# Kernel tuning notes

Hardware: AMD Instinct MI355X
Metric: run time of the kernel (lower is better)

Reference implementation:

```python
import jax, jax.numpy as jnp
import numpy as np

NUM_HEADS = 8
WINDOW_SIZE = 4
DIM = 384


def setup_inputs() -> dict:
    key = jax.random.key(0)
    k_x, k_qkv, k_pw, k_pb = jax.random.split(key, 4)
    B, N, C = 8, 16384, DIM
    x = jax.random.normal(k_x, (B, N, C), dtype=jnp.float32)
    # torch nn.Linear weights are [out_features, in_features]
    W_qkv = jax.random.normal(k_qkv, (3 * C, C), dtype=jnp.float32) * (1.0 / np.sqrt(C))
    W_proj = jax.random.normal(k_pw, (C, C), dtype=jnp.float32) * (1.0 / np.sqrt(C))
    b_proj = jax.random.normal(k_pb, (C,), dtype=jnp.float32) * 0.01
    return {"x": x, "W_qkv": W_qkv, "W_proj": W_proj, "b_proj": b_proj}


def reference(x, W_qkv, W_proj, b_proj):
    B, N, C = x.shape
    H = int(round(N ** 0.5))
    W = H
    ws = WINDOW_SIZE
    nh = NUM_HEADS
    hd = C // nh
    scale = hd ** -0.5
    hw, ww = H // ws, W // ws

    qkv = x @ W_qkv.T  # [B, N, 3C]
    qkv = qkv.reshape(B, N, 3, nh, hd)
    qkv = jnp.transpose(qkv, (2, 0, 3, 1, 4))  # [3, B, nh, N, hd]
    q, k, v = qkv[0], qkv[1], qkv[2]

    def to_windows(t):
        # [B, nh, N, hd] -> [B, nh, n_windows, ws*ws, hd]
        t = t.reshape(B, nh, hw, ws, ww, ws, hd)
        t = jnp.transpose(t, (0, 1, 2, 4, 3, 5, 6))
        return t.reshape(B, nh, hw * ww, ws * ws, hd)

    q, k, v = to_windows(q), to_windows(k), to_windows(v)

    attn = jnp.einsum('bhwqd,bhwkd->bhwqk', q, k) * scale
    attn = jax.nn.softmax(attn, axis=-1)
    out = jnp.einsum('bhwqk,bhwkd->bhwqd', attn, v)

    # windows back to [B, N, C]
    out = out.reshape(B, nh, hw, ww, ws, ws, hd)
    out = jnp.transpose(out, (0, 1, 2, 4, 3, 5, 6)).reshape(B, nh, N, hd)
    out = jnp.transpose(out, (0, 2, 1, 3)).reshape(B, N, C)

    out = out @ W_proj.T + b_proj
    return out
```

## Files before the change

### kernel.cpp

```cpp
#include <hip/hip_runtime.h>
#include <hip/hip_bf16.h>
#include <cstdint>

#define ASPACE(n) __attribute__((address_space(n)))

typedef short bf16x8 __attribute__((ext_vector_type(8)));
typedef float f32x4 __attribute__((ext_vector_type(4)));

__device__ __forceinline__ unsigned short f2bf(float f) {
  uint32_t u = __float_as_uint(f);
  u += 0x7fffu + ((u >> 16) & 1u);
  return (unsigned short)(u >> 16);
}
__device__ __forceinline__ float bf2f(unsigned short h) {
  return __uint_as_float(((uint32_t)h) << 16);
}

__global__ __launch_bounds__(256) void conv_f32_bf16(const float4* __restrict__ src,
                                                     ushort4* __restrict__ dst, int n4) {
  int i = blockIdx.x * blockDim.x + threadIdx.x;
  int stride = gridDim.x * blockDim.x;
  for (; i < n4; i += stride) {
    float4 v = src[i];
    ushort4 o;
    o.x = f2bf(v.x); o.y = f2bf(v.y); o.z = f2bf(v.z); o.w = f2bf(v.w);
    dst[i] = o;
  }
}

#define BM 128
#define BN 128
#define BKK 32

__device__ __forceinline__ void gload16(const unsigned short* g, unsigned short* l) {
  __builtin_amdgcn_global_load_lds((const ASPACE(1) void*)g, (ASPACE(3) void*)l, 16, 0, 0);
}

template <int OUT_MODE>
__global__ __launch_bounds__(256) void gemm_bt(const unsigned short* __restrict__ A,
                                               const unsigned short* __restrict__ B,
                                               void* __restrict__ Cout,
                                               const float* __restrict__ bias,
                                               int M, int N, int K) {
  __shared__ unsigned short As[BM * BKK];
  __shared__ unsigned short Bs[BN * BKK];
  const int tid  = threadIdx.x;
  const int lane = tid & 63;
  const int wave = tid >> 6;
  const int wr = wave >> 1, wc = wave & 1;
  const int bm0 = blockIdx.x * BM;
  const int bn0 = blockIdx.y * BN;

  f32x4 acc[4][4];
#pragma unroll
  for (int m = 0; m < 4; ++m)
#pragma unroll
    for (int n = 0; n < 4; ++n) {
      f32x4 z = {0.f, 0.f, 0.f, 0.f};
      acc[m][n] = z;
    }

  const int srow = lane >> 2;
  const int scol = (lane & 3) * 8;
  const int s0 = wave * 2, s1 = wave * 2 + 1;

  const unsigned short* Abase = A + (size_t)bm0 * K;
  const unsigned short* Bbase = B + (size_t)bn0 * K;

  const int fr   = lane & 15;
  const int koff = (lane >> 4) * 8;

  for (int k0 = 0; k0 < K; k0 += BKK) {
    gload16(Abase + (size_t)(s0 * 16 + srow) * K + k0 + scol, As + s0 * 512);
    gload16(Abase + (size_t)(s1 * 16 + srow) * K + k0 + scol, As + s1 * 512);
    gload16(Bbase + (size_t)(s0 * 16 + srow) * K + k0 + scol, Bs + s0 * 512);
    gload16(Bbase + (size_t)(s1 * 16 + srow) * K + k0 + scol, Bs + s1 * 512);
    __syncthreads();

    bf16x8 af[4], bfv[4];
#pragma unroll
    for (int m = 0; m < 4; ++m)
      af[m] = *(const bf16x8*)(As + (wr * 64 + m * 16 + fr) * BKK + koff);
#pragma unroll
    for (int n = 0; n < 4; ++n)
      bfv[n] = *(const bf16x8*)(Bs + (wc * 64 + n * 16 + fr) * BKK + koff);
#pragma unroll
    for (int m = 0; m < 4; ++m)
#pragma unroll
      for (int n = 0; n < 4; ++n)
        acc[m][n] = __builtin_amdgcn_mfma_f32_16x16x32_bf16(af[m], bfv[n], acc[m][n], 0, 0, 0);
    __syncthreads();
  }

  const int rq = (lane >> 4) * 4;
  if (OUT_MODE == 1) {
    float* C = (float*)Cout;
#pragma unroll
    for (int m = 0; m < 4; ++m) {
#pragma unroll
      for (int n = 0; n < 4; ++n) {
        int col = bn0 + wc * 64 + n * 16 + fr;
        float bv = bias[col];
#pragma unroll
        for (int r = 0; r < 4; ++r) {
          int row = bm0 + wr * 64 + m * 16 + rq + r;
          C[(size_t)row * N + col] = acc[m][n][r] + bv;
        }
      }
    }
  } else {
    unsigned short* C = (unsigned short*)Cout;
#pragma unroll
    for (int m = 0; m < 4; ++m) {
#pragma unroll
      for (int n = 0; n < 4; ++n) {
        int col = bn0 + wc * 64 + n * 16 + fr;
#pragma unroll
        for (int r = 0; r < 4; ++r) {
          int row = bm0 + wr * 64 + m * 16 + rq + r;
          C[(size_t)row * N + col] = f2bf(acc[m][n][r]);
        }
      }
    }
  }
}

#define PADV 24
#define PADP 24
__global__ __launch_bounds__(256) void win_attn(const unsigned short* __restrict__ qkv,
                                                unsigned short* __restrict__ aout) {
  __shared__ unsigned short lds[4][48 * PADV + 16 * PADP];
  const int tid = threadIdx.x;
  const int wave = tid >> 6, lane = tid & 63;
  const int wg = blockIdx.x * 4 + wave;
  const int h = wg & 7;
  const int bw = wg >> 3;
  const int w = bw & 1023, b = bw >> 10;
  const int wy = w >> 5, wx = w & 31;

  unsigned short* Vt = lds[wave];
  unsigned short* P  = lds[wave] + 48 * PADV;

  const int lg = lane >> 4;
  const int lr = lane & 15;

  const int n_lr = (wy * 4 + (lr >> 2)) * 128 + wx * 4 + (lr & 3);
  const size_t rowbase = ((size_t)(b * 16384 + n_lr)) * 1152 + h * 48;

  bf16x8 aq0, bk0;
  bf16x8 aq1 = {0, 0, 0, 0, 0, 0, 0, 0};
  bf16x8 bk1 = {0, 0, 0, 0, 0, 0, 0, 0};
  aq0 = *(const bf16x8*)(qkv + rowbase + lg * 8);
  bk0 = *(const bf16x8*)(qkv + rowbase + 384 + lg * 8);
  if (lg < 2) {
    aq1 = *(const bf16x8*)(qkv + rowbase + 32 + lg * 8);
    bk1 = *(const bf16x8*)(qkv + rowbase + 384 + 32 + lg * 8);
  }

  {
    bf16x8 v = *(const bf16x8*)(qkv + rowbase + 768 + lg * 8);
#pragma unroll
    for (int i = 0; i < 8; ++i) Vt[(lg * 8 + i) * PADV + lr] = (unsigned short)v[i];
    if (lane < 32) {
      bf16x8 v2 = *(const bf16x8*)(qkv + rowbase + 768 + 32 + lg * 8);
#pragma unroll
      for (int i = 0; i < 8; ++i) Vt[((4 + lg) * 8 + i) * PADV + lr] = (unsigned short)v2[i];
    }
  }

  f32x4 s = {0.f, 0.f, 0.f, 0.f};
  s = __builtin_amdgcn_mfma_f32_16x16x32_bf16(aq0, bk0, s, 0, 0, 0);
  s = __builtin_amdgcn_mfma_f32_16x16x32_bf16(aq1, bk1, s, 0, 0, 0);

  const float scale = 0.14433756729740643f;
  float p[4];
#pragma unroll
  for (int r = 0; r < 4; ++r) {
    float x = s[r] * scale;
    float m = x;
    m = fmaxf(m, __shfl_xor(m, 1));
    m = fmaxf(m, __shfl_xor(m, 2));
    m = fmaxf(m, __shfl_xor(m, 4));
    m = fmaxf(m, __shfl_xor(m, 8));
    float e = __expf(x - m);
    float t = e;
    t += __shfl_xor(t, 1);
    t += __shfl_xor(t, 2);
    t += __shfl_xor(t, 4);
    t += __shfl_xor(t, 8);
    p[r] = e / t;
  }
#pragma unroll
  for (int r = 0; r < 4; ++r) P[(lg * 4 + r) * PADP + lr] = f2bf(p[r]);

  __syncthreads();

  bf16x8 ap = {0, 0, 0, 0, 0, 0, 0, 0};
  if (lg < 2) ap = *(const bf16x8*)(P + lr * PADP + lg * 8);

  f32x4 o[3];
#pragma unroll
  for (int c = 0; c < 3; ++c) {
    bf16x8 bv = {0, 0, 0, 0, 0, 0, 0, 0};
    if (lg < 2) bv = *(const bf16x8*)(Vt + (c * 16 + lr) * PADV + lg * 8);
    f32x4 z = {0.f, 0.f, 0.f, 0.f};
    o[c] = __builtin_amdgcn_mfma_f32_16x16x32_bf16(ap, bv, z, 0, 0, 0);
  }

#pragma unroll
  for (int r = 0; r < 4; ++r) {
    const int qi = lg * 4 + r;
    const int nq = (wy * 4 + (qi >> 2)) * 128 + wx * 4 + (qi & 3);
    const size_t obase = ((size_t)(b * 16384 + nq)) * 384 + h * 48;
#pragma unroll
    for (int c = 0; c < 3; ++c)
      aout[obase + c * 16 + lr] = f2bf(o[c][r]);
  }
}

extern "C" void kernel_launch(void* const* d_in, const int* in_sizes, int n_in,
                              void* d_out, int out_size, void* d_ws, size_t ws_size,
                              hipStream_t stream) {
  const float* x      = (const float*)d_in[0];
  const float* W_qkv  = (const float*)d_in[1];
  const float* W_proj = (const float*)d_in[2];
  const float* b_proj = (const float*)d_in[3];
  float* out = (float*)d_out;

  const int Bb = 8, Nn = 16384, Cc = 384;
  const int M = Bb * Nn;
  const int threeC = 3 * Cc;

  char* ws = (char*)d_ws;
  unsigned short* qkv_bf  = (unsigned short*)ws;
  unsigned short* xa_bf   = (unsigned short*)(ws + (size_t)M * threeC * 2);
  unsigned short* wqkv_bf = (unsigned short*)(ws + (size_t)M * threeC * 2 + (size_t)M * Cc * 2);
  unsigned short* wproj_bf = wqkv_bf + threeC * Cc;

  conv_f32_bf16<<<2048, 256, 0, stream>>>((const float4*)x, (ushort4*)xa_bf, M * Cc / 4);
  conv_f32_bf16<<<432, 256, 0, stream>>>((const float4*)W_qkv, (ushort4*)wqkv_bf, threeC * Cc / 4);
  conv_f32_bf16<<<144, 256, 0, stream>>>((const float4*)W_proj, (ushort4*)wproj_bf, Cc * Cc / 4);

  dim3 g1(M / BM, threeC / BN);
  gemm_bt<0><<<g1, 256, 0, stream>>>(xa_bf, wqkv_bf, qkv_bf, nullptr, M, threeC, Cc);

  win_attn<<<Bb * 8 * 1024 / 4, 256, 0, stream>>>(qkv_bf, xa_bf);

  dim3 g2(M / BM, Cc / BN);
  gemm_bt<1><<<g2, 256, 0, stream>>>(xa_bf, wproj_bf, out, b_proj, M, Cc, Cc);
}
```

Baseline: 430.6 us.

## Double-buffer GEMM LDS tiles with BK=64, XOR swizzle and block remap

The GEMM now stages 64-wide K tiles into two LDS buffers, so the next tile's global-to-LDS load overlaps the MFMAs on the current one, and it halves the number of barriers. An XOR swizzle on the 16-byte chunk index is meant to avoid LDS bank conflicts on fragment reads. A 1-D grid is remapped across 8 groups to change the block visiting order and improve L2 reuse. LDS use rises to 64KB per block, which may lower occupancy.

```diff
diff --git a/kernel.cpp b/kernel.cpp
--- a/kernel.cpp
+++ b/kernel.cpp
@@ -28,12 +28,24 @@
   }
 }
 
-#define BM 128
-#define BN 128
-#define BKK 32
 
 __device__ __forceinline__ void gload16(const unsigned short* g, unsigned short* l) {
   __builtin_amdgcn_global_load_lds((const ASPACE(1) void*)g, (ASPACE(3) void*)l, 16, 0, 0);
+}
+
+__device__ __forceinline__ void stage_tile(const unsigned short* __restrict__ gbase, int K, int k0,
+                                           unsigned short* ldsbase, int wave, int lane) {
+#pragma unroll
+  for (int l = 0; l < 4; ++l) {
+    const int c = l * 256 + wave * 64 + lane;
+    const int r = c >> 3;
+    const int scc = (c & 7) ^ (r & 7);
+    gload16(gbase + (size_t)r * K + k0 + scc * 8, ldsbase + (l * 256 + wave * 64) * 8);
+  }
+}
+
+__device__ __forceinline__ bf16x8 frag_ld(const unsigned short* S, int row, int cb) {
+  return *(const bf16x8*)(S + row * 64 + ((cb ^ (row & 7)) * 8));
 }
 
 template <int OUT_MODE>
@@ -42,14 +54,22 @@
                                                void* __restrict__ Cout,
                                                const float* __restrict__ bias,
                                                int M, int N, int K) {
-  __shared__ unsigned short As[BM * BKK];
-  __shared__ unsigned short Bs[BN * BKK];
+  __shared__ unsigned short As[2][128 * 64];
+  __shared__ unsigned short Bs[2][128 * 64];
+
   const int tid  = threadIdx.x;
   const int lane = tid & 63;
   const int wave = tid >> 6;
   const int wr = wave >> 1, wc = wave & 1;
-  const int bm0 = blockIdx.x * BM;
-  const int bn0 = blockIdx.y * BN;
+
+  const int nwg = gridDim.x;
+  const int swz = (blockIdx.x & 7) * (nwg >> 3) + (blockIdx.x >> 3);
+  const int ntn = N >> 7;
+  const int bn0 = (swz % ntn) << 7;
+  const int bm0 = (swz / ntn) << 7;
+
+  const unsigned short* Abase = A + (size_t)bm0 * K;
+  const unsigned short* Bbase = B + (size_t)bn0 * K;
 
   f32x4 acc[4][4];
 #pragma unroll
@@ -60,39 +80,51 @@
       acc[m][n] = z;
     }
 
-  const int srow = lane >> 2;
-  const int scol = (lane & 3) * 8;
-  const int s0 = wave * 2, s1 = wave * 2 + 1;
-
-  const unsigned short* Abase = A + (size_t)bm0 * K;
-  const unsigned short* Bbase = B + (size_t)bn0 * K;
-
-  const int fr   = lane & 15;
-  const int koff = (lane >> 4) * 8;
-
-  for (int k0 = 0; k0 < K; k0 += BKK) {
-    gload16(Abase + (size_t)(s0 * 16 + srow) * K + k0 + scol, As + s0 * 512);
-    gload16(Abase + (size_t)(s1 * 16 + srow) * K + k0 + scol, As + s1 * 512);
-    gload16(Bbase + (size_t)(s0 * 16 + srow) * K + k0 + scol, Bs + s0 * 512);
-    gload16(Bbase + (size_t)(s1 * 16 + srow) * K + k0 + scol, Bs + s1 * 512);
+  const int fr = lane & 15;
+  const int hi = lane >> 4;
+  const int NT = K >> 6;
+
+  stage_tile(Abase, K, 0, As[0], wave, lane);
+  stage_tile(Bbase, K, 0, Bs[0], wave, lane);
+  __syncthreads();
+
+  int cur = 0;
+  for (int t = 0; t < NT - 1; ++t) {
+    stage_tile(Abase, K, (t + 1) << 6, As[cur ^ 1], wave, lane);
+    stage_tile(Bbase, K, (t + 1) << 6, Bs[cur ^ 1], wave, lane);
+#pragma unroll
+    for (int kk = 0; kk < 2; ++kk) {
+      bf16x8 af[4], bfv[4];
+      const int cb = kk * 4 + hi;
+#pragma unroll
+      for (int m = 0; m < 4; ++m) af[m] = frag_ld(As[cur], wr * 64 + m * 16 + fr, cb);
+#pragma unroll
+      for (int n = 0; n < 4; ++n) bfv[n] = frag_ld(Bs[cur], wc * 64 + n * 16 + fr, cb);
+#pragma unroll
+      for (int m = 0; m < 4; ++m)
+#pragma unroll
+        for (int n = 0; n < 4; ++n)
+          acc[m][n] = __builtin_amdgcn_mfma_f32_16x16x32_bf16(af[m], bfv[n], acc[m][n], 0, 0, 0);
+    }
     __syncthreads();
-
+    cur ^= 1;
+  }
+#pragma unroll
+  for (int kk = 0; kk < 2; ++kk) {
     bf16x8 af[4], bfv[4];
-#pragma unroll
-    for (int m = 0; m < 4; ++m)
-      af[m] = *(const bf16x8*)(As + (wr * 64 + m * 16 + fr) * BKK + koff);
-#pragma unroll
-    for (int n = 0; n < 4; ++n)
-      bfv[n] = *(const bf16x8*)(Bs + (wc * 64 + n * 16 + fr) * BKK + koff);
+    const int cb = kk * 4 + hi;
+#pragma unroll
+    for (int m = 0; m < 4; ++m) af[m] = frag_ld(As[cur], wr * 64 + m * 16 + fr, cb);
+#pragma unroll
+    for (int n = 0; n < 4; ++n) bfv[n] = frag_ld(Bs[cur], wc * 64 + n * 16 + fr, cb);
 #pragma unroll
     for (int m = 0; m < 4; ++m)
 #pragma unroll
       for (int n = 0; n < 4; ++n)
         acc[m][n] = __builtin_amdgcn_mfma_f32_16x16x32_bf16(af[m], bfv[n], acc[m][n], 0, 0, 0);
-    __syncthreads();
-  }
-
-  const int rq = (lane >> 4) * 4;
+  }
+
+  const int rq = hi * 4;
   if (OUT_MODE == 1) {
     float* C = (float*)Cout;
 #pragma unroll
@@ -241,11 +273,11 @@
   conv_f32_bf16<<<432, 256, 0, stream>>>((const float4*)W_qkv, (ushort4*)wqkv_bf, threeC * Cc / 4);
   conv_f32_bf16<<<144, 256, 0, stream>>>((const float4*)W_proj, (ushort4*)wproj_bf, Cc * Cc / 4);
 
-  dim3 g1(M / BM, threeC / BN);
-  gemm_bt<0><<<g1, 256, 0, stream>>>(xa_bf, wqkv_bf, qkv_bf, nullptr, M, threeC, Cc);
+  gemm_bt<0><<<(M / 128) * (threeC / 128), 256, 0, stream>>>(xa_bf, wqkv_bf, qkv_bf, nullptr,
+                                                             M, threeC, Cc);
 
   win_attn<<<Bb * 8 * 1024 / 4, 256, 0, stream>>>(qkv_bf, xa_bf);
 
-  dim3 g2(M / BM, Cc / BN);
-  gemm_bt<1><<<g2, 256, 0, stream>>>(xa_bf, wproj_bf, out, b_proj, M, Cc, Cc);
-}
+  gemm_bt<1><<<(M / 128) * (Cc / 128), 256, 0, stream>>>(xa_bf, wproj_bf, out, b_proj,
+                                                         M, Cc, Cc);
+}
```

Result: slower. 463.5 us (+7.6%).

## Keep full B panel resident in LDS and stream A fragments directly from global

Applied to the files above, without the earlier changes.

Replaces the per-K-step LDS-staged GEMM with a 512-thread kernel that loads a 128-column slice of the full K=384 weight panel into LDS once, then loops over several 256-row A tiles, reading A fragments straight from global memory into registers. Block indices are swizzled across groups of eight for locality. This removes the per-iteration barriers and A staging, and reuses the weight tile across multiple M tiles. In exchange it uses 96KB of LDS per block, which limits occupancy, and issues uncoalesced direct global A loads with no prefetch or double buffering.

```diff
diff --git a/kernel.cpp b/kernel.cpp
--- a/kernel.cpp
+++ b/kernel.cpp
@@ -1,8 +1,6 @@
 #include <hip/hip_runtime.h>
 #include <hip/hip_bf16.h>
 #include <cstdint>
-
-#define ASPACE(n) __attribute__((address_space(n)))
 
 typedef short bf16x8 __attribute__((ext_vector_type(8)));
 typedef float f32x4 __attribute__((ext_vector_type(4)));
@@ -28,99 +26,99 @@
   }
 }
 
-#define BM 128
-#define BN 128
-#define BKK 32
-
-__device__ __forceinline__ void gload16(const unsigned short* g, unsigned short* l) {
-  __builtin_amdgcn_global_load_lds((const ASPACE(1) void*)g, (ASPACE(3) void*)l, 16, 0, 0);
-}
 
 template <int OUT_MODE>
-__global__ __launch_bounds__(256) void gemm_bt(const unsigned short* __restrict__ A,
-                                               const unsigned short* __restrict__ B,
-                                               void* __restrict__ Cout,
-                                               const float* __restrict__ bias,
-                                               int M, int N, int K) {
-  __shared__ unsigned short As[BM * BKK];
-  __shared__ unsigned short Bs[BN * BKK];
+__global__ __launch_bounds__(512, 2) void gemm_bres(const unsigned short* __restrict__ A,
+                                                    const unsigned short* __restrict__ B,
+                                                    void* __restrict__ Cout,
+                                                    const float* __restrict__ bias,
+                                                    int M, int N, int ML) {
+  const int K = 384;
+  __shared__ unsigned short Bs[48 * 128 * 8];
+
   const int tid  = threadIdx.x;
   const int lane = tid & 63;
   const int wave = tid >> 6;
-  const int wr = wave >> 1, wc = wave & 1;
-  const int bm0 = blockIdx.x * BM;
-  const int bn0 = blockIdx.y * BN;
-
-  f32x4 acc[4][4];
-#pragma unroll
-  for (int m = 0; m < 4; ++m)
-#pragma unroll
-    for (int n = 0; n < 4; ++n) {
-      f32x4 z = {0.f, 0.f, 0.f, 0.f};
-      acc[m][n] = z;
-    }
-
-  const int srow = lane >> 2;
-  const int scol = (lane & 3) * 8;
-  const int s0 = wave * 2, s1 = wave * 2 + 1;
-
-  const unsigned short* Abase = A + (size_t)bm0 * K;
+
+  const int nwg = gridDim.x;
+  const int swz = ((blockIdx.x & 7) * (nwg >> 3)) + (blockIdx.x >> 3);
+  const int ntn = N >> 7;
+  const int jb = swz % ntn;
+  const int g  = swz / ntn;
+  const int bn0 = jb << 7;
+
   const unsigned short* Bbase = B + (size_t)bn0 * K;
 
-  const int fr   = lane & 15;
-  const int koff = (lane >> 4) * 8;
-
-  for (int k0 = 0; k0 < K; k0 += BKK) {
-    gload16(Abase + (size_t)(s0 * 16 + srow) * K + k0 + scol, As + s0 * 512);
-    gload16(Abase + (size_t)(s1 * 16 + srow) * K + k0 + scol, As + s1 * 512);
-    gload16(Bbase + (size_t)(s0 * 16 + srow) * K + k0 + scol, Bs + s0 * 512);
-    gload16(Bbase + (size_t)(s1 * 16 + srow) * K + k0 + scol, Bs + s1 * 512);
-    __syncthreads();
-
-    bf16x8 af[4], bfv[4];
-#pragma unroll
-    for (int m = 0; m < 4; ++m)
-      af[m] = *(const bf16x8*)(As + (wr * 64 + m * 16 + fr) * BKK + koff);
-#pragma unroll
-    for (int n = 0; n < 4; ++n)
-      bfv[n] = *(const bf16x8*)(Bs + (wc * 64 + n * 16 + fr) * BKK + koff);
-#pragma unroll
-    for (int m = 0; m < 4; ++m)
-#pragma unroll
-      for (int n = 0; n < 4; ++n)
-        acc[m][n] = __builtin_amdgcn_mfma_f32_16x16x32_bf16(af[m], bfv[n], acc[m][n], 0, 0, 0);
-    __syncthreads();
-  }
-
-  const int rq = (lane >> 4) * 4;
-  if (OUT_MODE == 1) {
-    float* C = (float*)Cout;
-#pragma unroll
-    for (int m = 0; m < 4; ++m) {
-#pragma unroll
-      for (int n = 0; n < 4; ++n) {
-        int col = bn0 + wc * 64 + n * 16 + fr;
-        float bv = bias[col];
-#pragma unroll
-        for (int r = 0; r < 4; ++r) {
-          int row = bm0 + wr * 64 + m * 16 + rq + r;
-          C[(size_t)row * N + col] = acc[m][n][r] + bv;
+  {
+    const int br = tid >> 2;
+    const int bj = tid & 3;
+#pragma unroll
+    for (int i = 0; i < 12; ++i) {
+      const int cc = bj + 4 * i;
+      bf16x8 t = *(const bf16x8*)(Bbase + (size_t)br * K + cc * 8);
+      *(bf16x8*)(Bs + (cc * 128 + br) * 8) = t;
+    }
+  }
+  __syncthreads();
+
+  const int fr = lane & 15;
+  const int hi = lane >> 4;
+
+  for (int mt = 0; mt < ML; ++mt) {
+    const int bm = (g * ML + mt) * 256;
+    const unsigned short* Arow = A + (size_t)(bm + wave * 32 + fr) * K + hi * 8;
+
+    f32x4 acc[2][8];
+#pragma unroll
+    for (int mf = 0; mf < 2; ++mf)
+#pragma unroll
+      for (int nf = 0; nf < 8; ++nf) {
+        f32x4 z = {0.f, 0.f, 0.f, 0.f};
+        acc[mf][nf] = z;
+      }
+
+#pragma unroll
+    for (int ks = 0; ks < 12; ++ks) {
+      bf16x8 af0 = *(const bf16x8*)(Arow + ks * 32);
+      bf16x8 af1 = *(const bf16x8*)(Arow + (size_t)16 * K + ks * 32);
+      bf16x8 bfv[8];
+#pragma unroll
+      for (int nf = 0; nf < 8; ++nf)
+        bfv[nf] = *(const bf16x8*)(Bs + ((ks * 4 + hi) * 128 + nf * 16 + fr) * 8);
+#pragma unroll
+      for (int nf = 0; nf < 8; ++nf) {
+        acc[0][nf] = __builtin_amdgcn_mfma_f32_16x16x32_bf16(af0, bfv[nf], acc[0][nf], 0, 0, 0);
+        acc[1][nf] = __builtin_amdgcn_mfma_f32_16x16x32_bf16(af1, bfv[nf], acc[1][nf], 0, 0, 0);
+      }
+    }
+
+    if (OUT_MODE == 1) {
+      float* C = (float*)Cout;
+#pragma unroll
+      for (int mf = 0; mf < 2; ++mf)
+#pragma unroll
+        for (int nf = 0; nf < 8; ++nf) {
+          const int col = bn0 + nf * 16 + fr;
+          const float bv = bias[col];
+#pragma unroll
+          for (int r = 0; r < 4; ++r) {
+            const int row = bm + wave * 32 + mf * 16 + hi * 4 + r;
+            C[(size_t)row * N + col] = acc[mf][nf][r] + bv;
+          }
         }
-      }
-    }
-  } else {
-    unsigned short* C = (unsigned short*)Cout;
-#pragma unroll
-    for (int m = 0; m < 4; ++m) {
-#pragma unroll
-      for (int n = 0; n < 4; ++n) {
-        int col = bn0 + wc * 64 + n * 16 + fr;
-#pragma unroll
-        for (int r = 0; r < 4; ++r) {
-          int row = bm0 + wr * 64 + m * 16 + rq + r;
-          C[(size_t)row * N + col] = f2bf(acc[m][n][r]);
+    } else {
+      unsigned short* C = (unsigned short*)Cout;
+#pragma unroll
+      for (int mf = 0; mf < 2; ++mf)
+#pragma unroll
+        for (int nf = 0; nf < 8; ++nf) {
+          const int col = bn0 + nf * 16 + fr;
+#pragma unroll
+          for (int r = 0; r < 4; ++r) {
+            const int row = bm + wave * 32 + mf * 16 + hi * 4 + r;
+            C[(size_t)row * N + col] = f2bf(acc[mf][nf][r]);
+          }
         }
-      }
     }
   }
 }
@@ -241,11 +239,12 @@
   conv_f32_bf16<<<432, 256, 0, stream>>>((const float4*)W_qkv, (ushort4*)wqkv_bf, threeC * Cc / 4);
   conv_f32_bf16<<<144, 256, 0, stream>>>((const float4*)W_proj, (ushort4*)wproj_bf, Cc * Cc / 4);
 
-  dim3 g1(M / BM, threeC / BN);
-  gemm_bt<0><<<g1, 256, 0, stream>>>(xa_bf, wqkv_bf, qkv_bf, nullptr, M, threeC, Cc);
+  const int ML = 2;
+  gemm_bres<0><<<(M / (256 * ML)) * (threeC / 128), 512, 0, stream>>>(
+      xa_bf, wqkv_bf, qkv_bf, nullptr, M, threeC, ML);
 
   win_attn<<<Bb * 8 * 1024 / 4, 256, 0, stream>>>(qkv_bf, xa_bf);
 
-  dim3 g2(M / BM, Cc / BN);
-  gemm_bt<1><<<g2, 256, 0, stream>>>(xa_bf, wproj_bf, out, b_proj, M, Cc, Cc);
-}
+  gemm_bres<1><<<(M / (256 * ML)) * (Cc / 128), 512, 0, stream>>>(
+      xa_bf, wproj_bf, out, b_proj, M, Cc, ML);
+}
```

Measured after the change: 1.237 ms. +187.2%, slower.
